# Optimization experiments

Measured on AMD Instinct MI355X. Metric: run time of the kernel, lower is better.

The kernel has to match this reference:

```python
import jax, jax.numpy as jnp
import numpy as np

TAU = 0.5
LOGIT_TAU = float(np.log(TAU / (1.0 - TAU)))  # = 0.0 for tau=0.5
N_STEPS = 128           # torch samples randint(128,129) -> always 128
N_SECANT = 8
D_MIN, D_MAX = 0.0, 2.4
B, N, HID, CDIM = 4, 8192, 64, 128


def decoder(p, c, W1, Wc, b1, W2, b2):
    """Occupancy-logit MLP. p: (B, ..., 3), c: (B, CDIM) -> (B, ...)."""
    cc = c @ Wc  # (B, HID)
    cc = cc.reshape(cc.shape[:1] + (1,) * (p.ndim - 2) + cc.shape[1:])
    h = jax.nn.relu(jnp.einsum('...d,dh->...h', p, W1) + cc + b1)
    return (h @ W2 + b2)[..., 0]


def setup_inputs() -> dict:
    key = jax.random.key(0)
    ks = jax.random.split(key, 8)
    return {
        'ray0': jax.random.normal(ks[0], (B, N, 3), jnp.float32) * 0.5,
        'ray_direction': jax.random.normal(ks[1], (B, N, 3), jnp.float32),
        'c': jax.random.normal(ks[2], (B, CDIM), jnp.float32),
        'W1': jax.random.normal(ks[3], (3, HID), jnp.float32) * 0.5,
        'Wc': jax.random.normal(ks[4], (CDIM, HID), jnp.float32) * 0.1,
        'b1': jax.random.normal(ks[5], (HID,), jnp.float32) * 0.1,
        'W2': jax.random.normal(ks[6], (HID, 1), jnp.float32) * 0.5,
        'b2': jax.random.normal(ks[7], (1,), jnp.float32) * 0.1,
    }


def reference(ray0, ray_direction, c, W1, Wc, b1, W2, b2):
    S = N_STEPS
    bsz, npts, _ = ray0.shape
    dec = lambda p: decoder(p, c, W1, Wc, b1, W2, b2)

    # --- coarse ray marching ---
    d_prop = jnp.linspace(D_MIN, D_MAX, S).astype(ray0.dtype)        # (S,)
    p_prop = ray0[:, :, None, :] + ray_direction[:, :, None, :] * d_prop[None, None, :, None]
    val = dec(p_prop) - LOGIT_TAU                                    # (B, N, S)

    mask_0_not_occupied = val[:, :, 0] < 0
    sign_matrix = jnp.concatenate(
        [jnp.sign(val[:, :, :-1] * val[:, :, 1:]),
         jnp.ones((bsz, npts, 1), val.dtype)], axis=-1)
    cost_matrix = sign_matrix * jnp.arange(S, 0, -1, dtype=val.dtype)
    indices = jnp.argmin(cost_matrix, axis=-1)                       # (B, N)
    values = jnp.min(cost_matrix, axis=-1)
    mask_sign_change = values < 0
    f_low = jnp.take_along_axis(val, indices[..., None], axis=2)[..., 0]
    mask_neg_to_pos = f_low < 0
    mask = mask_sign_change & mask_neg_to_pos & mask_0_not_occupied

    d_prop_full = jnp.broadcast_to(d_prop, (bsz, npts, S))
    d_low = jnp.take_along_axis(d_prop_full, indices[..., None], axis=2)[..., 0]
    idx_hi = jnp.minimum(indices + 1, S - 1)
    d_high = jnp.take_along_axis(d_prop_full, idx_hi[..., None], axis=2)[..., 0]
    f_high = jnp.take_along_axis(val, idx_hi[..., None], axis=2)[..., 0]

    # safe placeholders for non-surface rays (results discarded by mask)
    d_low = jnp.where(mask, d_low, 0.0)
    d_high = jnp.where(mask, d_high, 1.0)
    f_low = jnp.where(mask, f_low, -1.0)
    f_high = jnp.where(mask, f_high, 1.0)

    # --- secant refinement (vectorized over all rays) ---
    d_pred = -f_low * (d_high - d_low) / (f_high - f_low) + d_low
    for _ in range(N_SECANT):
        p_mid = ray0 + d_pred[..., None] * ray_direction
        f_mid = dec(p_mid) - LOGIT_TAU
        ind_low = f_mid < 0
        d_low = jnp.where(ind_low, d_pred, d_low)
        f_low = jnp.where(ind_low, f_mid, f_low)
        d_high = jnp.where(ind_low, d_high, d_pred)
        f_high = jnp.where(ind_low, f_high, f_mid)
        d_pred = -f_low * (d_high - d_low) / (f_high - f_low) + d_low

    d_out = jnp.where(mask, d_pred, jnp.inf)
    d_out = jnp.where(mask_0_not_occupied, d_out, 0.0)
    return d_out
```

## Files before the change

kernel.cpp:

```cpp
#include <hip/hip_runtime.h>
#include <hip/hip_bf16.h>

#define HID   64
#define CDIM  128
#define NSTEP 128
#define NRAYS 32768

typedef const __hip_bfloat16* __restrict__ bf16p;
typedef float v2f __attribute__((ext_vector_type(2)));

#define WS_CCB 0
#define WS_WX  256
#define WS_WY  320
#define WS_WZ  384
#define WS_W2  448

__device__ __forceinline__ float bf2f(__hip_bfloat16 x) { return __bfloat162float(x); }

#if __has_builtin(__builtin_elementwise_fma)
__device__ __forceinline__ v2f vfma2(v2f a, v2f b, v2f c) { return __builtin_elementwise_fma(a, b, c); }
#else
__device__ __forceinline__ v2f vfma2(v2f a, v2f b, v2f c) {
    v2f r; r.x = fmaf(a.x, b.x, c.x); r.y = fmaf(a.y, b.y, c.y); return r;
}
#endif
#if __has_builtin(__builtin_elementwise_max)
__device__ __forceinline__ v2f vmax2(v2f a, v2f b) { return __builtin_elementwise_max(a, b); }
#else
__device__ __forceinline__ v2f vmax2(v2f a, v2f b) {
    v2f r; r.x = fmaxf(a.x, b.x); r.y = fmaxf(a.y, b.y); return r;
}
#endif
__device__ __forceinline__ v2f splat2(float s) { v2f v; v.x = s; v.y = s; return v; }

__global__ void precompute_cc(bf16p c, bf16p Wc, bf16p b1, bf16p W1, bf16p W2,
                              float* __restrict__ ws) {
    __shared__ float part[4][HID];
    int b = blockIdx.x;
    int h = threadIdx.x & 63;
    int q = threadIdx.x >> 6;
    float acc = 0.0f;
    const __hip_bfloat16* crow = c + b * CDIM;
#pragma unroll
    for (int k = q * 32; k < q * 32 + 32; ++k)
        acc = fmaf(bf2f(crow[k]), bf2f(Wc[k * HID + h]), acc);
    part[q][h] = acc;
    if (b == 0) {
        if (q == 1) {
            ws[WS_WX + h] = bf2f(W1[h]);
            ws[WS_WY + h] = bf2f(W1[HID + h]);
        } else if (q == 2) {
            ws[WS_WZ + h] = bf2f(W1[2 * HID + h]);
            ws[WS_W2 + h] = bf2f(W2[h]);
        }
    }
    __syncthreads();
    if (q == 0)
        ws[WS_CCB + b * HID + h] =
            bf2f(b1[h]) + ((part[0][h] + part[1][h]) + (part[2][h] + part[3][h]));
}

__global__ __launch_bounds__(256) void raymarch(
    bf16p ray0, bf16p rdir, bf16p b2,
    const float* __restrict__ ws, __hip_bfloat16* __restrict__ out) {
    const int tid  = threadIdx.x;
    const int wave = tid >> 6;
    const int lane = tid & 63;
    const int r    = blockIdx.x * 4 + wave;
    const int batch = blockIdx.x >> 11;

    const float slx = ws[WS_WX + lane];
    const float sly = ws[WS_WY + lane];
    const float slz = ws[WS_WZ + lane];
    const float sl2 = ws[WS_W2 + lane];
    const float scb = ws[WS_CCB + batch * HID + lane];

    const float b2v = bf2f(b2[0]);
    const float ox = bf2f(ray0[r * 3 + 0]), oy = bf2f(ray0[r * 3 + 1]), oz = bf2f(ray0[r * 3 + 2]);
    const float dx = bf2f(rdir[r * 3 + 0]), dy = bf2f(rdir[r * 3 + 1]), dz = bf2f(rdir[r * 3 + 2]);

    const float STEPF = 2.4f / 127.0f;
    const float d0 = bf2f(__float2bfloat16(lane * STEPF));
    const float d1 = bf2f(__float2bfloat16((lane + 64) * STEPF));

    const float px0 = fmaf(d0, dx, ox), py0 = fmaf(d0, dy, oy), pz0 = fmaf(d0, dz, oz);
    const float px1 = fmaf(d1, dx, ox), py1 = fmaf(d1, dy, oy), pz1 = fmaf(d1, dz, oz);

    const v2f px0v = splat2(px0), py0v = splat2(py0), pz0v = splat2(pz0);
    const v2f px1v = splat2(px1), py1v = splat2(py1), pz1v = splat2(pz1);
    const v2f zero2 = splat2(0.0f);

    const v2f* __restrict__ WX2 = (const v2f*)(ws + WS_WX);
    const v2f* __restrict__ WY2 = (const v2f*)(ws + WS_WY);
    const v2f* __restrict__ WZ2 = (const v2f*)(ws + WS_WZ);
    const v2f* __restrict__ W22 = (const v2f*)(ws + WS_W2);
    const v2f* __restrict__ CB2 = (const v2f*)(ws + WS_CCB + batch * HID);

    v2f acc0; acc0.x = b2v; acc0.y = 0.0f;
    v2f acc1 = acc0;
#pragma unroll 8
    for (int q = 0; q < HID / 2; ++q) {
        const v2f wx = WX2[q], wy = WY2[q], wz = WZ2[q], w2 = W22[q], cb = CB2[q];
        v2f h0 = vfma2(px0v, wx, vfma2(py0v, wy, vfma2(pz0v, wz, cb)));
        v2f h1 = vfma2(px1v, wx, vfma2(py1v, wy, vfma2(pz1v, wz, cb)));
        h0 = vmax2(h0, zero2);
        h1 = vmax2(h1, zero2);
        acc0 = vfma2(h0, w2, acc0);
        acc1 = vfma2(h1, w2, acc1);
    }
    float val0 = acc0.x + acc0.y;
    float val1 = acc1.x + acc1.y;

    float v1l0  = __shfl(val1, 0);
    float valn0 = __shfl_down(val0, 1);
    valn0 = (lane == 63) ? v1l0 : valn0;
    float valn1 = __shfl_down(val1, 1);

    float prod0 = val0 * valn0;
    float sgn0  = (prod0 < 0.0f) ? -1.0f : ((prod0 > 0.0f) ? 1.0f : 0.0f);
    float cost0 = sgn0 * (float)(128 - lane);

    float prod1 = val1 * valn1;
    float sgn1  = (prod1 < 0.0f) ? -1.0f : ((prod1 > 0.0f) ? 1.0f : 0.0f);
    float cost1 = (lane == 63) ? 1.0f
                               : sgn1 * (float)(64 - lane);

    float key0 = fmaf(cost0, 256.0f, (float)lane);
    float key1 = fmaf(cost1, 256.0f, (float)(lane + 64));
    float k = fminf(key0, key1);
#pragma unroll
    for (int off = 32; off > 0; off >>= 1)
        k = fminf(k, __shfl_xor(k, off));
    const float cf = floorf(k * 0.00390625f);
    const int   mi = (int)(k - cf * 256.0f);

    const int idx  = mi;
    const int idxh = (idx + 1 < NSTEP) ? idx + 1 : NSTEP - 1;

    float va  = __shfl(val0, idx  & 63);
    float vb  = __shfl(val1, idx  & 63);
    float f_low  = (idx  < 64) ? va  : vb;
    float vah = __shfl(val0, idxh & 63);
    float vbh = __shfl(val1, idxh & 63);
    float f_high = (idxh < 64) ? vah : vbh;

    float v00 = __shfl(val0, 0);
    bool  m0   = v00 < 0.0f;
    bool  mask = (cf < 0.0f) && (f_low < 0.0f) && m0;

    float result;
    if (mask) {
        float dl = bf2f(__float2bfloat16(idx  * STEPF));
        float dh = bf2f(__float2bfloat16(idxh * STEPF));
        float fl = f_low, fh = f_high;
        float dp = -fl * (dh - dl) / (fh - fl) + dl;
#pragma unroll
        for (int it = 0; it < 8; ++it) {
            float px = fmaf(dp, dx, ox), py = fmaf(dp, dy, oy), pz = fmaf(dp, dz, oz);
            float h = fmaf(px, slx, fmaf(py, sly, fmaf(pz, slz, scb)));
            h = fmaxf(h, 0.0f);
            float t = h * sl2;
            for (int off = 32; off > 0; off >>= 1) t += __shfl_xor(t, off);
            float fm = t + b2v;
            bool lowside = fm < 0.0f;
            dl = lowside ? dp : dl;
            fl = lowside ? fm : fl;
            dh = lowside ? dh : dp;
            fh = lowside ? fh : fm;
            dp = -fl * (dh - dl) / (fh - fl) + dl;
        }
        result = dp;
    } else {
        result = m0 ? 0x1.FEp127f : 0.0f;
    }
    if (lane == 0) out[r] = __float2bfloat16(result);
}

extern "C" void kernel_launch(void* const* d_in, const int* in_sizes, int n_in,
                              void* d_out, int out_size, void* d_ws, size_t ws_size,
                              hipStream_t stream) {
    bf16p ray0 = (bf16p)d_in[0];
    bf16p rdir = (bf16p)d_in[1];
    bf16p c    = (bf16p)d_in[2];
    bf16p W1   = (bf16p)d_in[3];
    bf16p Wc   = (bf16p)d_in[4];
    bf16p b1   = (bf16p)d_in[5];
    bf16p W2   = (bf16p)d_in[6];
    bf16p b2   = (bf16p)d_in[7];
    __hip_bfloat16* out = (__hip_bfloat16*)d_out;
    float* ws = (float*)d_ws;

    hipLaunchKernelGGL(precompute_cc, dim3(4), dim3(256), 0, stream, c, Wc, b1, W1, W2, ws);
    hipLaunchKernelGGL(raymarch, dim3(NRAYS / 4), dim3(256), 0, stream,
                       ray0, rdir, b2, ws, out);
}
```

Before: 99.58 us.

## Use fp16 dot2 for coarse MLP and compact secant rays into separate kernel

The coarse march now packs (px,py) and (pz,1) into half2 and evaluates the first layer with v_dot2 instructions against packed fp16 weights and bias, halving the FMA count per hidden unit. Rays that need refinement are appended to per-batch queues with an atomic counter, and a new secant kernel handles them one thread per ray, replacing the wave-wide shuffle reductions run by every wave. This removes divergence and reduction overhead from secant, but adds an extra launch, atomics, workspace traffic, and fp16 rounding of positions and weights, which can shift sign changes.

```diff
diff --git a/kernel.cpp b/kernel.cpp
--- a/kernel.cpp
+++ b/kernel.cpp
@@ -7,31 +7,31 @@
 #define NRAYS 32768
 
 typedef const __hip_bfloat16* __restrict__ bf16p;
-typedef float v2f __attribute__((ext_vector_type(2)));
-
-#define WS_CCB 0
-#define WS_WX  256
-#define WS_WY  320
-#define WS_WZ  384
-#define WS_W2  448
+typedef _Float16 h2 __attribute__((ext_vector_type(2)));
+
+#define WS_CCB  0
+#define WS_WX   256
+#define WS_WY   320
+#define WS_WZ   384
+#define WS_W2   448
+#define WS_CNT  512
+#define WS_WXY  520
+#define WS_WZCB 584
+#define QID     1024
+#define QDL     (QID + 32768)
+#define QDH     (QDL + 32768)
+#define QFL     (QDH + 32768)
+#define QFH     (QFL + 32768)
 
 __device__ __forceinline__ float bf2f(__hip_bfloat16 x) { return __bfloat162float(x); }
 
-#if __has_builtin(__builtin_elementwise_fma)
-__device__ __forceinline__ v2f vfma2(v2f a, v2f b, v2f c) { return __builtin_elementwise_fma(a, b, c); }
-#else
-__device__ __forceinline__ v2f vfma2(v2f a, v2f b, v2f c) {
-    v2f r; r.x = fmaf(a.x, b.x, c.x); r.y = fmaf(a.y, b.y, c.y); return r;
-}
-#endif
-#if __has_builtin(__builtin_elementwise_max)
-__device__ __forceinline__ v2f vmax2(v2f a, v2f b) { return __builtin_elementwise_max(a, b); }
-#else
-__device__ __forceinline__ v2f vmax2(v2f a, v2f b) {
-    v2f r; r.x = fmaxf(a.x, b.x); r.y = fmaxf(a.y, b.y); return r;
-}
-#endif
-__device__ __forceinline__ v2f splat2(float s) { v2f v; v.x = s; v.y = s; return v; }
+__device__ __forceinline__ unsigned pack_h2(float a, float b) {
+    h2 v; v.x = (_Float16)a; v.y = (_Float16)b;
+    union { h2 h; unsigned u; } c; c.h = v; return c.u;
+}
+__device__ __forceinline__ h2 as_h2(unsigned u) {
+    union { unsigned u; h2 h; } c; c.u = u; return c.h;
+}
 
 __global__ void precompute_cc(bf16p c, bf16p Wc, bf16p b1, bf16p W1, bf16p W2,
                               float* __restrict__ ws) {
@@ -47,37 +47,37 @@
     part[q][h] = acc;
     if (b == 0) {
         if (q == 1) {
-            ws[WS_WX + h] = bf2f(W1[h]);
-            ws[WS_WY + h] = bf2f(W1[HID + h]);
+            float wx = bf2f(W1[h]), wy = bf2f(W1[HID + h]);
+            ws[WS_WX + h] = wx;
+            ws[WS_WY + h] = wy;
+            ((unsigned*)ws)[WS_WXY + h] = pack_h2(wx, wy);
         } else if (q == 2) {
             ws[WS_WZ + h] = bf2f(W1[2 * HID + h]);
             ws[WS_W2 + h] = bf2f(W2[h]);
+        } else if (q == 3 && h < 4) {
+            ((int*)ws)[WS_CNT + h] = 0;
         }
     }
     __syncthreads();
+    float cb = bf2f(b1[h]) + ((part[0][h] + part[1][h]) + (part[2][h] + part[3][h]));
     if (q == 0)
-        ws[WS_CCB + b * HID + h] =
-            bf2f(b1[h]) + ((part[0][h] + part[1][h]) + (part[2][h] + part[3][h]));
+        ws[WS_CCB + b * HID + h] = cb;
+    else if (q == 1)
+        ((unsigned*)ws)[WS_WZCB + b * HID + h] = pack_h2(bf2f(W1[2 * HID + h]), cb);
 }
 
 __global__ __launch_bounds__(256) void raymarch(
     bf16p ray0, bf16p rdir, bf16p b2,
-    const float* __restrict__ ws, __hip_bfloat16* __restrict__ out) {
+    float* __restrict__ ws, __hip_bfloat16* __restrict__ out) {
     const int tid  = threadIdx.x;
     const int wave = tid >> 6;
     const int lane = tid & 63;
     const int r    = blockIdx.x * 4 + wave;
     const int batch = blockIdx.x >> 11;
 
-    const float slx = ws[WS_WX + lane];
-    const float sly = ws[WS_WY + lane];
-    const float slz = ws[WS_WZ + lane];
-    const float sl2 = ws[WS_W2 + lane];
-    const float scb = ws[WS_CCB + batch * HID + lane];
-
-    const float b2v = bf2f(b2[0]);
     const float ox = bf2f(ray0[r * 3 + 0]), oy = bf2f(ray0[r * 3 + 1]), oz = bf2f(ray0[r * 3 + 2]);
     const float dx = bf2f(rdir[r * 3 + 0]), dy = bf2f(rdir[r * 3 + 1]), dz = bf2f(rdir[r * 3 + 2]);
+    const float b2v = bf2f(b2[0]);
 
     const float STEPF = 2.4f / 127.0f;
     const float d0 = bf2f(__float2bfloat16(lane * STEPF));
@@ -86,30 +86,53 @@
     const float px0 = fmaf(d0, dx, ox), py0 = fmaf(d0, dy, oy), pz0 = fmaf(d0, dz, oz);
     const float px1 = fmaf(d1, dx, ox), py1 = fmaf(d1, dy, oy), pz1 = fmaf(d1, dz, oz);
 
-    const v2f px0v = splat2(px0), py0v = splat2(py0), pz0v = splat2(pz0);
-    const v2f px1v = splat2(px1), py1v = splat2(py1), pz1v = splat2(pz1);
-    const v2f zero2 = splat2(0.0f);
-
-    const v2f* __restrict__ WX2 = (const v2f*)(ws + WS_WX);
-    const v2f* __restrict__ WY2 = (const v2f*)(ws + WS_WY);
-    const v2f* __restrict__ WZ2 = (const v2f*)(ws + WS_WZ);
-    const v2f* __restrict__ W22 = (const v2f*)(ws + WS_W2);
-    const v2f* __restrict__ CB2 = (const v2f*)(ws + WS_CCB + batch * HID);
-
-    v2f acc0; acc0.x = b2v; acc0.y = 0.0f;
-    v2f acc1 = acc0;
+    float val0, val1;
+#if __has_builtin(__builtin_amdgcn_fdot2)
+    {
+        const h2 pxy0 = as_h2(pack_h2(px0, py0));
+        const h2 pxy1 = as_h2(pack_h2(px1, py1));
+        const h2 pz0o = as_h2(pack_h2(pz0, 1.0f));
+        const h2 pz1o = as_h2(pack_h2(pz1, 1.0f));
+        const unsigned* __restrict__ WXY  = (const unsigned*)ws + WS_WXY;
+        const unsigned* __restrict__ WZCB = (const unsigned*)ws + WS_WZCB + batch * HID;
+        const float* __restrict__ W2F = ws + WS_W2;
+        float a0 = b2v, a1 = 0.0f, a2 = 0.0f, a3 = 0.0f;
 #pragma unroll 8
-    for (int q = 0; q < HID / 2; ++q) {
-        const v2f wx = WX2[q], wy = WY2[q], wz = WZ2[q], w2 = W22[q], cb = CB2[q];
-        v2f h0 = vfma2(px0v, wx, vfma2(py0v, wy, vfma2(pz0v, wz, cb)));
-        v2f h1 = vfma2(px1v, wx, vfma2(py1v, wy, vfma2(pz1v, wz, cb)));
-        h0 = vmax2(h0, zero2);
-        h1 = vmax2(h1, zero2);
-        acc0 = vfma2(h0, w2, acc0);
-        acc1 = vfma2(h1, w2, acc1);
-    }
-    float val0 = acc0.x + acc0.y;
-    float val1 = acc1.x + acc1.y;
+        for (int j = 0; j < HID; j += 2) {
+            h2 wxyA = as_h2(WXY[j]),     wxyB = as_h2(WXY[j + 1]);
+            h2 wzcA = as_h2(WZCB[j]),    wzcB = as_h2(WZCB[j + 1]);
+            float w2A = W2F[j], w2B = W2F[j + 1];
+            float hA0 = __builtin_amdgcn_fdot2(pxy0, wxyA, __builtin_amdgcn_fdot2(pz0o, wzcA, 0.0f, false), false);
+            float hA1 = __builtin_amdgcn_fdot2(pxy1, wxyA, __builtin_amdgcn_fdot2(pz1o, wzcA, 0.0f, false), false);
+            float hB0 = __builtin_amdgcn_fdot2(pxy0, wxyB, __builtin_amdgcn_fdot2(pz0o, wzcB, 0.0f, false), false);
+            float hB1 = __builtin_amdgcn_fdot2(pxy1, wxyB, __builtin_amdgcn_fdot2(pz1o, wzcB, 0.0f, false), false);
+            a0 = fmaf(fmaxf(hA0, 0.0f), w2A, a0);
+            a1 = fmaf(fmaxf(hA1, 0.0f), w2A, a1);
+            a2 = fmaf(fmaxf(hB0, 0.0f), w2B, a2);
+            a3 = fmaf(fmaxf(hB1, 0.0f), w2B, a3);
+        }
+        val0 = a0 + a2;
+        val1 = (a1 + a3) + b2v;
+    }
+#else
+    {
+        const float* __restrict__ WXF = ws + WS_WX;
+        const float* __restrict__ WYF = ws + WS_WY;
+        const float* __restrict__ WZF = ws + WS_WZ;
+        const float* __restrict__ W2F = ws + WS_W2;
+        const float* __restrict__ CBF = ws + WS_CCB + batch * HID;
+        float a0 = b2v, a1 = b2v;
+#pragma unroll 8
+        for (int j = 0; j < HID; ++j) {
+            float wx = WXF[j], wy = WYF[j], wz = WZF[j], w2 = W2F[j], cb = CBF[j];
+            float h0 = fmaf(px0, wx, fmaf(py0, wy, fmaf(pz0, wz, cb)));
+            float h1 = fmaf(px1, wx, fmaf(py1, wy, fmaf(pz1, wz, cb)));
+            a0 = fmaf(fmaxf(h0, 0.0f), w2, a0);
+            a1 = fmaf(fmaxf(h1, 0.0f), w2, a1);
+        }
+        val0 = a0; val1 = a1;
+    }
+#endif
 
     float v1l0  = __shfl(val1, 0);
     float valn0 = __shfl_down(val0, 1);
@@ -119,11 +142,9 @@
     float prod0 = val0 * valn0;
     float sgn0  = (prod0 < 0.0f) ? -1.0f : ((prod0 > 0.0f) ? 1.0f : 0.0f);
     float cost0 = sgn0 * (float)(128 - lane);
-
     float prod1 = val1 * valn1;
     float sgn1  = (prod1 < 0.0f) ? -1.0f : ((prod1 > 0.0f) ? 1.0f : 0.0f);
-    float cost1 = (lane == 63) ? 1.0f
-                               : sgn1 * (float)(64 - lane);
+    float cost1 = (lane == 63) ? 1.0f : sgn1 * (float)(64 - lane);
 
     float key0 = fmaf(cost0, 256.0f, (float)lane);
     float key1 = fmaf(cost1, 256.0f, (float)(lane + 64));
@@ -148,32 +169,63 @@
     bool  m0   = v00 < 0.0f;
     bool  mask = (cf < 0.0f) && (f_low < 0.0f) && m0;
 
-    float result;
-    if (mask) {
-        float dl = bf2f(__float2bfloat16(idx  * STEPF));
-        float dh = bf2f(__float2bfloat16(idxh * STEPF));
-        float fl = f_low, fh = f_high;
-        float dp = -fl * (dh - dl) / (fh - fl) + dl;
+    if (lane == 0) {
+        if (mask) {
+            int pos = atomicAdd((int*)ws + WS_CNT + batch, 1);
+            int qo  = batch * 8192 + pos;
+            ((int*)ws)[QID + qo] = r;
+            ws[QDL + qo] = bf2f(__float2bfloat16(idx  * STEPF));
+            ws[QDH + qo] = bf2f(__float2bfloat16(idxh * STEPF));
+            ws[QFL + qo] = f_low;
+            ws[QFH + qo] = f_high;
+        } else {
+            out[r] = __float2bfloat16(m0 ? 0x1.FEp127f : 0.0f);
+        }
+    }
+}
+
+__global__ __launch_bounds__(256) void secant(
+    bf16p ray0, bf16p rdir, bf16p b2,
+    const float* __restrict__ ws, __hip_bfloat16* __restrict__ out) {
+    const int gtid  = blockIdx.x * 256 + threadIdx.x;
+    const int batch = gtid >> 13;
+    const int i     = gtid & 8191;
+    const int cnt   = ((const int*)ws)[WS_CNT + batch];
+    if (i >= cnt) return;
+
+    const int qo  = batch * 8192 + i;
+    const int rid = ((const int*)ws)[QID + qo];
+    float dl = ws[QDL + qo], dh = ws[QDH + qo];
+    float fl = ws[QFL + qo], fh = ws[QFH + qo];
+
+    const float ox = bf2f(ray0[rid * 3 + 0]), oy = bf2f(ray0[rid * 3 + 1]), oz = bf2f(ray0[rid * 3 + 2]);
+    const float dx = bf2f(rdir[rid * 3 + 0]), dy = bf2f(rdir[rid * 3 + 1]), dz = bf2f(rdir[rid * 3 + 2]);
+    const float b2v = bf2f(b2[0]);
+
+    const float* __restrict__ WXF = ws + WS_WX;
+    const float* __restrict__ WYF = ws + WS_WY;
+    const float* __restrict__ WZF = ws + WS_WZ;
+    const float* __restrict__ W2F = ws + WS_W2;
+    const float* __restrict__ CBF = ws + WS_CCB + batch * HID;
+
+    float dp = -fl * (dh - dl) / (fh - fl) + dl;
 #pragma unroll
-        for (int it = 0; it < 8; ++it) {
-            float px = fmaf(dp, dx, ox), py = fmaf(dp, dy, oy), pz = fmaf(dp, dz, oz);
-            float h = fmaf(px, slx, fmaf(py, sly, fmaf(pz, slz, scb)));
-            h = fmaxf(h, 0.0f);
-            float t = h * sl2;
-            for (int off = 32; off > 0; off >>= 1) t += __shfl_xor(t, off);
-            float fm = t + b2v;
-            bool lowside = fm < 0.0f;
-            dl = lowside ? dp : dl;
-            fl = lowside ? fm : fl;
-            dh = lowside ? dh : dp;
-            fh = lowside ? fh : fm;
-            dp = -fl * (dh - dl) / (fh - fl) + dl;
-        }
-        result = dp;
-    } else {
-        result = m0 ? 0x1.FEp127f : 0.0f;
-    }
-    if (lane == 0) out[r] = __float2bfloat16(result);
+    for (int it = 0; it < 8; ++it) {
+        float px = fmaf(dp, dx, ox), py = fmaf(dp, dy, oy), pz = fmaf(dp, dz, oz);
+        float acc = b2v;
+#pragma unroll 8
+        for (int j = 0; j < HID; ++j) {
+            float h = fmaf(px, WXF[j], fmaf(py, WYF[j], fmaf(pz, WZF[j], CBF[j])));
+            acc = fmaf(fmaxf(h, 0.0f), W2F[j], acc);
+        }
+        bool lowside = acc < 0.0f;
+        dl = lowside ? dp : dl;
+        fl = lowside ? acc : fl;
+        dh = lowside ? dh : dp;
+        fh = lowside ? fh : acc;
+        dp = -fl * (dh - dl) / (fh - fl) + dl;
+    }
+    out[rid] = __float2bfloat16(dp);
 }
 
 extern "C" void kernel_launch(void* const* d_in, const int* in_sizes, int n_in,
@@ -193,4 +245,6 @@
     hipLaunchKernelGGL(precompute_cc, dim3(4), dim3(256), 0, stream, c, Wc, b1, W1, W2, ws);
     hipLaunchKernelGGL(raymarch, dim3(NRAYS / 4), dim3(256), 0, stream,
                        ray0, rdir, b2, ws, out);
-}
+    hipLaunchKernelGGL(secant, dim3(128), dim3(256), 0, stream,
+                       ray0, rdir, b2, ws, out);
+}
```

Result: slower. 110.0 us (+10.5%).
